# Optimization experiments

Measured on AMD Instinct MI355X. Metric: run time of the kernel, lower is better.

The kernel has to match this reference:

```python
import jax, jax.numpy as jnp
import numpy as np

H = 8        # num_heads
LN_EPS = 1e-5
NEG = -1000000.0


def setup_inputs() -> dict:
    key = jax.random.key(0)
    ks = jax.random.split(key, 8)
    B, T, D = 4, 4096, 1024
    s = 1.0 / np.sqrt(D)
    x = jax.random.normal(ks[0], (B, T, D), dtype=jnp.float32)
    tmask = (jnp.arange(T) < (3 * T) // 4).astype(jnp.float32)
    src_mask = jnp.broadcast_to(tmask[None, :, None], (B, T, 1)).astype(jnp.float32)
    Wq = jax.random.normal(ks[1], (D, D), dtype=jnp.float32) * s
    Wk = jax.random.normal(ks[2], (D, D), dtype=jnp.float32) * s
    Wv = jax.random.normal(ks[3], (D, D), dtype=jnp.float32) * s
    bq = jnp.zeros((D,), jnp.float32)
    bk = jnp.zeros((D,), jnp.float32)
    bv = jnp.zeros((D,), jnp.float32)
    gamma = jnp.ones((D,), jnp.float32)
    beta = jnp.zeros((D,), jnp.float32)
    return {"x": x, "src_mask": src_mask, "Wq": Wq, "bq": bq, "Wk": Wk,
            "bk": bk, "Wv": Wv, "bv": bv, "gamma": gamma, "beta": beta}


def reference(x, src_mask, Wq, bq, Wk, bk, Wv, bv, gamma, beta):
    B, T, D = x.shape
    Dh = D // H
    # LayerNorm (same normed input feeds q, k, v)
    mu = jnp.mean(x, axis=-1, keepdims=True)
    var = jnp.mean(jnp.square(x - mu), axis=-1, keepdims=True)
    xn = (x - mu) * jax.lax.rsqrt(var + LN_EPS) * gamma + beta
    q = xn @ Wq + bq                               # [B,T,D]
    k = xn @ Wk + bk + (1.0 - src_mask) * NEG      # mask padded timesteps
    v = (xn @ Wv + bv) * src_mask                  # zero padded values
    q = jax.nn.softmax(q.reshape(B, T, H, Dh), axis=-1)   # over feature dim
    k = jax.nn.softmax(k.reshape(B, T, H, Dh), axis=1)    # over time dim
    v = v.reshape(B, T, H, Dh)
    # efficient/linear attention: O(T * Dh^2) per head
    att = jnp.einsum('bnhd,bnhl->bhdl', k, v)      # [B,H,Dh,Dh]
    y = jnp.einsum('bnhd,bhdl->bnhl', q, att).reshape(B, T, D)
    return x + y
```

## Files before the change

### kernel.cpp

```cpp
#include <hip/hip_runtime.h>
#include <stdint.h>


typedef unsigned short u16;
typedef __attribute__((ext_vector_type(8))) short bf16x8;
typedef __attribute__((ext_vector_type(4))) float f32x4;

__device__ u16 g_WT[3][1024 * 1024];
__device__ u16 g_xn[16777216];
__device__ u16 g_ekT[16777216];
__device__ u16 g_vvT[16777216];
__device__ float g_attp[8388608];
__device__ u16 g_attT[524288];
__device__ float g_Z[4096];

__device__ __forceinline__ float b2f(u16 u) {
  union { unsigned int i; float f; } c;
  c.i = ((unsigned int)u) << 16;
  return c.f;
}
__device__ __forceinline__ u16 f2b(float f) {
  union { float f; unsigned int i; } c;
  c.f = f;
  unsigned int r = c.i + 0x7fffu + ((c.i >> 16) & 1u);
  return (u16)(r >> 16);
}

__device__ __forceinline__ void gload16(const void* g, void* l) {
  __builtin_amdgcn_global_load_lds(
      reinterpret_cast<const __attribute__((address_space(1))) uint32_t*>(
          reinterpret_cast<uintptr_t>(g)),
      reinterpret_cast<__attribute__((address_space(3))) uint32_t*>(
          reinterpret_cast<uintptr_t>(l)),
      16, 0, 0);
}

__device__ __forceinline__ void stage128x32(const u16* g, int stride, char* lds,
                                            int wave, int lane) {
  const int r = wave * 32 + (lane >> 2);
  const int cb = (lane & 3) * 16;
  const char* gp = (const char*)g;
  gload16(gp + (size_t)r * stride * 2 + cb, lds + wave * 2048);
  gload16(gp + (size_t)(r + 16) * stride * 2 + cb, lds + wave * 2048 + 1024);
}

__device__ __forceinline__ bf16x8 frag_ld(const char* lds, int row, int lane) {
  return *(const bf16x8*)(lds + row * 64 + ((lane >> 4) * 16));
}

__device__ __forceinline__ void tile_mfma(const char* As, const char* Bs,
                                          f32x4 (&acc)[4][4], int wm, int wn,
                                          int lane) {
  bf16x8 af[4], bfr[4];
#pragma unroll
  for (int i = 0; i < 4; i++) af[i] = frag_ld(As, wm * 64 + i * 16 + (lane & 15), lane);
#pragma unroll
  for (int j = 0; j < 4; j++) bfr[j] = frag_ld(Bs, wn * 64 + j * 16 + (lane & 15), lane);
#pragma unroll
  for (int i = 0; i < 4; i++)
#pragma unroll
    for (int j = 0; j < 4; j++)
      acc[i][j] = __builtin_amdgcn_mfma_f32_16x16x32_bf16(af[i], bfr[j], acc[i][j], 0, 0, 0);
}

__global__ __launch_bounds__(256) void prep_kernel(const float* __restrict__ x,
                                                   const float* __restrict__ gamma,
                                                   const float* __restrict__ beta,
                                                   const float* __restrict__ wq,
                                                   const float* __restrict__ wk,
                                                   const float* __restrict__ wv) {
  __shared__ float ls[4], ls2[4];
  __shared__ u16 tile[32][33];
  const int bid = blockIdx.x;
  const int tid = threadIdx.x;
  if (bid < 16384) {
    if (bid < 16) g_Z[bid * 256 + tid] = 0.0f;
    const int wave = tid >> 6, lane = tid & 63;
    const float* xr = x + (size_t)bid * 1024;
    float4 u = ((const float4*)xr)[tid];
    float v0 = u.x, v1 = u.y, v2 = u.z, v3 = u.w;
    float s = v0 + v1 + v2 + v3;
    float s2 = v0 * v0 + v1 * v1 + v2 * v2 + v3 * v3;
#pragma unroll
    for (int off = 32; off > 0; off >>= 1) {
      s += __shfl_down(s, off);
      s2 += __shfl_down(s2, off);
    }
    if (lane == 0) { ls[wave] = s; ls2[wave] = s2; }
    __syncthreads();
    s = ls[0] + ls[1] + ls[2] + ls[3];
    s2 = ls2[0] + ls2[1] + ls2[2] + ls2[3];
    const float mu = s * (1.0f / 1024.0f);
    const float var = fmaxf(s2 * (1.0f / 1024.0f) - mu * mu, 0.0f);
    const float rstd = rsqrtf(var + 1e-5f);
    float4 g4 = ((const float4*)gamma)[tid];
    float4 be = ((const float4*)beta)[tid];
    ushort4 o;
    o.x = f2b((v0 - mu) * rstd * g4.x + be.x);
    o.y = f2b((v1 - mu) * rstd * g4.y + be.y);
    o.z = f2b((v2 - mu) * rstd * g4.z + be.z);
    o.w = f2b((v3 - mu) * rstd * g4.w + be.w);
    *(ushort4*)(g_xn + (size_t)bid * 1024 + tid * 4) = o;
  } else {
    const int id = bid - 16384;
    const int which = id >> 10;
    const int rem = id & 1023;
    const float* src = (which == 0) ? wq : (which == 1) ? wk : wv;
    u16* dst = g_WT[which];
    const int tx = tid & 31;
    const int ty = tid >> 5;
    const int c0 = (rem & 31) * 32, r0 = (rem >> 5) * 32;
#pragma unroll
    for (int i = 0; i < 4; i++)
      tile[ty + i * 8][tx] = f2b(src[(size_t)(r0 + ty + i * 8) * 1024 + c0 + tx]);
    __syncthreads();
#pragma unroll
    for (int i = 0; i < 4; i++)
      dst[(size_t)(c0 + ty + i * 8) * 1024 + r0 + tx] = tile[tx][ty + i * 8];
  }
}

__global__ __launch_bounds__(256) void gemm_kv(const float* __restrict__ bk,
                                               const float* __restrict__ bv,
                                               const float* __restrict__ mask) {
  __shared__ __align__(16) char smem[34816];
  char* A0 = smem;
  char* B0 = smem + 8192;
  char* A1 = smem + 16384;
  char* B1 = smem + 24576;
  u16* tT = (u16*)smem;
  const int tid = threadIdx.x, wave = tid >> 6, lane = tid & 63;
  const int L = blockIdx.x;
  const int c = L & 7;
  const int k = L >> 3;
  const int inner = k & 15;
  const int n0 = (inner & 7) * 128;
  const int z = inner >> 3;
  const int m0 = (c + 8 * (k >> 4)) * 128;
  const u16* wt = z ? g_WT[2] : g_WT[1];
  const float* bias = z ? bv : bk;
  u16* outT = z ? g_vvT : g_ekT;
  const int b = m0 >> 12;
  const int t0 = m0 & 4095;
  const int wm = wave & 1, wn = wave >> 1;
  const u16* Ag = g_xn + (size_t)m0 * 1024;
  const u16* Bg = wt + (size_t)n0 * 1024;

  f32x4 zero = {0.f, 0.f, 0.f, 0.f};
  f32x4 acc[4][4];
#pragma unroll
  for (int i = 0; i < 4; i++)
#pragma unroll
    for (int j = 0; j < 4; j++) acc[i][j] = zero;

  stage128x32(Ag, 1024, A0, wave, lane);
  stage128x32(Bg, 1024, B0, wave, lane);
  __syncthreads();
  for (int k0 = 0; k0 < 1024; k0 += 64) {
    stage128x32(Ag + k0 + 32, 1024, A1, wave, lane);
    stage128x32(Bg + k0 + 32, 1024, B1, wave, lane);
    tile_mfma(A0, B0, acc, wm, wn, lane);
    __syncthreads();
    if (k0 + 64 < 1024) {
      stage128x32(Ag + k0 + 64, 1024, A0, wave, lane);
      stage128x32(Bg + k0 + 64, 1024, B0, wave, lane);
    }
    tile_mfma(A1, B1, acc, wm, wn, lane);
    __syncthreads();
  }

  float fsum[4] = {0.f, 0.f, 0.f, 0.f};
#pragma unroll
  for (int i = 0; i < 4; i++)
#pragma unroll
    for (int r = 0; r < 4; r++) {
      const int rowl = wm * 64 + i * 16 + (lane >> 4) * 4 + r;
      const float mv = mask[m0 + rowl];
#pragma unroll
      for (int j = 0; j < 4; j++) {
        const int coll = wn * 64 + j * 16 + (lane & 15);
        const float a = acc[i][j][r] + bias[n0 + coll];
        float o;
        if (z)
          o = a * mv;
        else
          o = (mv > 0.5f) ? __expf(fminf(a, 30.0f)) : 0.0f;
        const u16 ob = f2b(o);
        tT[coll * 136 + rowl] = ob;
        if (!z) fsum[j] += b2f(ob);
      }
    }
  if (!z) {
#pragma unroll
    for (int j = 0; j < 4; j++) {
      float s = fsum[j];
      s += __shfl_xor(s, 16);
      s += __shfl_xor(s, 32);
      if (lane < 16) atomicAdd(&g_Z[b * 1024 + n0 + wn * 64 + j * 16 + lane], s);
    }
  }
  __syncthreads();
  const size_t gbase = (size_t)b * (1024 * 4096) + (size_t)n0 * 4096 + t0;
#pragma unroll
  for (int u = 0; u < 8; u++) {
    const int v = u * 256 + tid;
    const int cc = v >> 4, rb = (v & 15) * 8;
    uint4 val = *(const uint4*)&tT[cc * 136 + rb];
    *(uint4*)(outT + gbase + (size_t)cc * 4096 + rb) = val;
  }
}

__global__ __launch_bounds__(256) void gemm_att() {
  __shared__ __align__(16) char smem[32768];
  char* A0 = smem;
  char* B0 = smem + 8192;
  char* A1 = smem + 16384;
  char* B1 = smem + 24576;
  const int tid = threadIdx.x, wave = tid >> 6, lane = tid & 63;
  const int kc = blockIdx.x;
  const int bh = blockIdx.y;
  const int b = bh >> 3, h = bh & 7;
  const size_t base = (size_t)b * (1024 * 4096) + (size_t)(h * 128) * 4096;
  const int wm = wave & 1, wn = wave >> 1;
  const u16* Ag = g_ekT + base + kc * 256;
  const u16* Bg = g_vvT + base + kc * 256;

  f32x4 zero = {0.f, 0.f, 0.f, 0.f};
  f32x4 acc[4][4];
#pragma unroll
  for (int i = 0; i < 4; i++)
#pragma unroll
    for (int j = 0; j < 4; j++) acc[i][j] = zero;

  stage128x32(Ag, 4096, A0, wave, lane);
  stage128x32(Bg, 4096, B0, wave, lane);
  __syncthreads();
  for (int kt = 0; kt < 256; kt += 64) {
    stage128x32(Ag + kt + 32, 4096, A1, wave, lane);
    stage128x32(Bg + kt + 32, 4096, B1, wave, lane);
    tile_mfma(A0, B0, acc, wm, wn, lane);
    __syncthreads();
    if (kt + 64 < 256) {
      stage128x32(Ag + kt + 64, 4096, A0, wave, lane);
      stage128x32(Bg + kt + 64, 4096, B0, wave, lane);
    }
    tile_mfma(A1, B1, acc, wm, wn, lane);
    __syncthreads();
  }

  float* op = g_attp + ((size_t)(kc * 32 + bh)) * 16384;
#pragma unroll
  for (int i = 0; i < 4; i++)
#pragma unroll
    for (int r = 0; r < 4; r++) {
      const int row = wm * 64 + i * 16 + (lane >> 4) * 4 + r;
#pragma unroll
      for (int j = 0; j < 4; j++) {
        const int col = wn * 64 + j * 16 + (lane & 15);
        op[row * 128 + col] = acc[i][j][r];
      }
    }
}

__global__ __launch_bounds__(256) void attnorm_kernel() {
  const int bh = blockIdx.x;
  const int b = bh >> 3, h = bh & 7;
  const int tid = threadIdx.x;
  __shared__ float Zl[128];
  if (tid < 128) Zl[tid] = fmaxf(g_Z[b * 1024 + h * 128 + tid], 1e-30f);
  __syncthreads();
  const int i0 = blockIdx.y * 2048;
  for (int i = i0 + tid; i < i0 + 2048; i += 256) {
    const int d = i >> 7, l = i & 127;
    float s = 0.f;
#pragma unroll
    for (int c = 0; c < 16; c++) s += g_attp[((size_t)(c * 32 + bh)) * 16384 + i];
    g_attT[(size_t)bh * 16384 + l * 128 + d] = f2b(s / Zl[d]);
  }
}

__global__ __launch_bounds__(256) void gemm_qy(const float* __restrict__ bq,
                                               const float* __restrict__ x,
                                               float* __restrict__ out) {
  __shared__ __align__(16) char smem[51200];
  __shared__ float zqp[2][128];
  char* A0 = smem;
  char* B0 = smem + 8192;
  char* A1 = smem + 16384;
  char* B1 = smem + 24576;
  u16* qs = (u16*)smem;
  char* C0 = smem + 34816;
  char* C1 = smem + 43008;
  const int tid = threadIdx.x, wave = tid >> 6, lane = tid & 63;
  const int L = blockIdx.x;
  const int c = L & 7;
  const int k = L >> 3;
  const int h = k & 7;
  const int m0 = (c + 8 * (k >> 3)) * 128;
  const int b = m0 >> 12;
  const int bh = b * 8 + h;
  const int wm = wave & 1, wn = wave >> 1;
  const u16* Ag = g_xn + (size_t)m0 * 1024;
  const u16* Bg = g_WT[0] + (size_t)(h * 128) * 1024;
  const u16* Cg = g_attT + (size_t)bh * 16384;

  f32x4 zero = {0.f, 0.f, 0.f, 0.f};
  f32x4 acc[4][4];
#pragma unroll
  for (int i = 0; i < 4; i++)
#pragma unroll
    for (int j = 0; j < 4; j++) acc[i][j] = zero;

  stage128x32(Ag, 1024, A0, wave, lane);
  stage128x32(Bg, 1024, B0, wave, lane);
  __syncthreads();
  for (int k0 = 0; k0 < 1024; k0 += 64) {
    stage128x32(Ag + k0 + 32, 1024, A1, wave, lane);
    stage128x32(Bg + k0 + 32, 1024, B1, wave, lane);
    tile_mfma(A0, B0, acc, wm, wn, lane);
    __syncthreads();
    if (k0 + 64 < 1024) {
      stage128x32(Ag + k0 + 64, 1024, A0, wave, lane);
      stage128x32(Bg + k0 + 64, 1024, B0, wave, lane);
    }
    tile_mfma(A1, B1, acc, wm, wn, lane);
    __syncthreads();
  }

  stage128x32(Cg, 128, C0, wave, lane);

#pragma unroll
  for (int i = 0; i < 4; i++)
#pragma unroll
    for (int r = 0; r < 4; r++) {
      const int rowl = wm * 64 + i * 16 + (lane >> 4) * 4 + r;
      float rs = 0.f;
#pragma unroll
      for (int j = 0; j < 4; j++) {
        const int coll = wn * 64 + j * 16 + (lane & 15);
        const float e = __expf(fminf(acc[i][j][r] + bq[h * 128 + coll], 30.0f));
        qs[rowl * 136 + coll] = f2b(e);
        rs += e;
      }
      rs += __shfl_xor(rs, 1);
      rs += __shfl_xor(rs, 2);
      rs += __shfl_xor(rs, 4);
      rs += __shfl_xor(rs, 8);
      if ((lane & 15) == 0) zqp[wn][rowl] = rs;
    }
  __syncthreads();

  f32x4 acc2[4][4];
#pragma unroll
  for (int i = 0; i < 4; i++)
#pragma unroll
    for (int j = 0; j < 4; j++) acc2[i][j] = zero;

  for (int k0 = 0; k0 < 128; k0 += 64) {
    stage128x32(Cg + k0 + 32, 128, C1, wave, lane);
    {
      bf16x8 af[4], bfr[4];
#pragma unroll
      for (int i = 0; i < 4; i++)
        af[i] = *(const bf16x8*)&qs[(wm * 64 + i * 16 + (lane & 15)) * 136 + k0 + (lane >> 4) * 8];
#pragma unroll
      for (int j = 0; j < 4; j++) bfr[j] = frag_ld(C0, wn * 64 + j * 16 + (lane & 15), lane);
#pragma unroll
      for (int i = 0; i < 4; i++)
#pragma unroll
        for (int j = 0; j < 4; j++)
          acc2[i][j] = __builtin_amdgcn_mfma_f32_16x16x32_bf16(af[i], bfr[j], acc2[i][j], 0, 0, 0);
    }
    __syncthreads();
    if (k0 + 64 < 128) stage128x32(Cg + k0 + 64, 128, C0, wave, lane);
    {
      bf16x8 af[4], bfr[4];
#pragma unroll
      for (int i = 0; i < 4; i++)
        af[i] = *(const bf16x8*)&qs[(wm * 64 + i * 16 + (lane & 15)) * 136 + k0 + 32 + (lane >> 4) * 8];
#pragma unroll
      for (int j = 0; j < 4; j++) bfr[j] = frag_ld(C1, wn * 64 + j * 16 + (lane & 15), lane);
#pragma unroll
      for (int i = 0; i < 4; i++)
#pragma unroll
        for (int j = 0; j < 4; j++)
          acc2[i][j] = __builtin_amdgcn_mfma_f32_16x16x32_bf16(af[i], bfr[j], acc2[i][j], 0, 0, 0);
    }
    __syncthreads();
  }

#pragma unroll
  for (int i = 0; i < 4; i++)
#pragma unroll
    for (int r = 0; r < 4; r++) {
      const int rowl = wm * 64 + i * 16 + (lane >> 4) * 4 + r;
      const float zq = fmaxf(zqp[0][rowl] + zqp[1][rowl], 1e-30f);
      const size_t n = (size_t)m0 + rowl;
#pragma unroll
      for (int j = 0; j < 4; j++) {
        const int coll = wn * 64 + j * 16 + (lane & 15);
        const size_t idx = n * 1024 + h * 128 + coll;
        out[idx] = x[idx] + acc2[i][j][r] / zq;
      }
    }
}

extern "C" void kernel_launch(void* const* d_in, const int* in_sizes, int n_in,
                              void* d_out, int out_size, void* d_ws, size_t ws_size,
                              hipStream_t stream) {
  const float* x = (const float*)d_in[0];
  const float* mask = (const float*)d_in[1];
  const float* Wq = (const float*)d_in[2];
  const float* bq = (const float*)d_in[3];
  const float* Wk = (const float*)d_in[4];
  const float* bk = (const float*)d_in[5];
  const float* Wv = (const float*)d_in[6];
  const float* bv = (const float*)d_in[7];
  const float* gamma = (const float*)d_in[8];
  const float* beta = (const float*)d_in[9];
  float* out = (float*)d_out;
  (void)d_ws; (void)ws_size;

  prep_kernel<<<dim3(16384 + 3072), 256, 0, stream>>>(x, gamma, beta, Wq, Wk, Wv);
  gemm_kv<<<dim3(2048), 256, 0, stream>>>(bk, bv, mask);
  gemm_att<<<dim3(16, 32), 256, 0, stream>>>();
  attnorm_kernel<<<dim3(32, 8), 256, 0, stream>>>();
  gemm_qy<<<dim3(1024), 256, 0, stream>>>(bq, x, out);
}
```

Before: 378.0 us.

## Rewrite K/V GEMM with 256x256 tiles, 8 waves, swizzled LDS, pipelined stages

The K/V projection GEMM moves from 128x128 tiles with 4 waves to 256x256 tiles with 8 waves (512 threads). It uses 128 KB of XOR-swizzled shared memory, double-buffered with explicit vmcnt waits, barriers and setprio around interleaved MFMA phases. The aim is more operand reuse per loaded byte, fewer LDS bank conflicts, and loads overlapped with MFMA work. The cost is much higher LDS and register use per block, lower occupancy, and 512 blocks that may fill the GPU's CUs less evenly.

```diff
diff --git a/kernel.cpp b/kernel.cpp
--- a/kernel.cpp
+++ b/kernel.cpp
@@ -61,6 +61,35 @@
 #pragma unroll
     for (int j = 0; j < 4; j++)
       acc[i][j] = __builtin_amdgcn_mfma_f32_16x16x32_bf16(af[i], bfr[j], acc[i][j], 0, 0, 0);
+}
+
+__device__ __forceinline__ void stageA256(char* buf, const u16* gsrc, int h,
+                                          int wave, int lane) {
+#pragma unroll
+  for (int i = 0; i < 2; i++) {
+    const int ib = i * 64 + wave * 8;
+    const int rowb = (ib & 63) | ((ib & 64) << 1) | (h << 6);
+    const int row = rowb + (lane >> 3);
+    const int cc = (lane & 7) ^ (row & 7);
+    gload16((const char*)gsrc + ((size_t)row * 1024 + cc * 8) * 2,
+            buf + rowb * 128);
+  }
+}
+__device__ __forceinline__ void stageB256(char* buf, const u16* gsrc, int h,
+                                          int wave, int lane) {
+#pragma unroll
+  for (int i = 0; i < 2; i++) {
+    const int ib = i * 64 + wave * 8;
+    const int rowb = (ib & 31) | ((ib & 96) << 1) | (h << 5);
+    const int row = rowb + (lane >> 3);
+    const int cc = (lane & 7) ^ (row & 7);
+    gload16((const char*)gsrc + ((size_t)row * 1024 + cc * 8) * 2,
+            buf + rowb * 128);
+  }
+}
+__device__ __forceinline__ bf16x8 fragS(const char* buf, int R, int ks, int lane) {
+  const int q = lane >> 4;
+  return *(const bf16x8*)(buf + R * 128 + ((((ks << 2) + q) ^ (R & 7)) << 4));
 }
 
 __global__ __launch_bounds__(256) void prep_kernel(const float* __restrict__ x,
@@ -120,93 +149,190 @@
   }
 }
 
-__global__ __launch_bounds__(256) void gemm_kv(const float* __restrict__ bk,
-                                               const float* __restrict__ bv,
-                                               const float* __restrict__ mask) {
-  __shared__ __align__(16) char smem[34816];
-  char* A0 = smem;
-  char* B0 = smem + 8192;
-  char* A1 = smem + 16384;
-  char* B1 = smem + 24576;
-  u16* tT = (u16*)smem;
+__global__ __launch_bounds__(512, 2) void gemm_kv(const float* __restrict__ bk,
+                                                  const float* __restrict__ bv,
+                                                  const float* __restrict__ mask) {
+  __shared__ __align__(16) char smem[131072];
   const int tid = threadIdx.x, wave = tid >> 6, lane = tid & 63;
   const int L = blockIdx.x;
-  const int c = L & 7;
-  const int k = L >> 3;
-  const int inner = k & 15;
-  const int n0 = (inner & 7) * 128;
-  const int z = inner >> 3;
-  const int m0 = (c + 8 * (k >> 4)) * 128;
+  const int mt = (L & 7) + 8 * (L >> 6);
+  const int nt = (L >> 3) & 7;
+  const int n0 = (nt & 3) * 256;
+  const int z = nt >> 2;
+  const int m0 = mt * 256;
   const u16* wt = z ? g_WT[2] : g_WT[1];
   const float* bias = z ? bv : bk;
   u16* outT = z ? g_vvT : g_ekT;
   const int b = m0 >> 12;
   const int t0 = m0 & 4095;
-  const int wm = wave & 1, wn = wave >> 1;
+  const int wm = wave >> 2, wn = wave & 3;
   const u16* Ag = g_xn + (size_t)m0 * 1024;
   const u16* Bg = wt + (size_t)n0 * 1024;
 
   f32x4 zero = {0.f, 0.f, 0.f, 0.f};
-  f32x4 acc[4][4];
-#pragma unroll
-  for (int i = 0; i < 4; i++)
+  f32x4 acc[8][4];
+#pragma unroll
+  for (int i = 0; i < 8; i++)
 #pragma unroll
     for (int j = 0; j < 4; j++) acc[i][j] = zero;
-
-  stage128x32(Ag, 1024, A0, wave, lane);
-  stage128x32(Bg, 1024, B0, wave, lane);
-  __syncthreads();
-  for (int k0 = 0; k0 < 1024; k0 += 64) {
-    stage128x32(Ag + k0 + 32, 1024, A1, wave, lane);
-    stage128x32(Bg + k0 + 32, 1024, B1, wave, lane);
-    tile_mfma(A0, B0, acc, wm, wn, lane);
-    __syncthreads();
-    if (k0 + 64 < 1024) {
-      stage128x32(Ag + k0 + 64, 1024, A0, wave, lane);
-      stage128x32(Bg + k0 + 64, 1024, B0, wave, lane);
-    }
-    tile_mfma(A1, B1, acc, wm, wn, lane);
-    __syncthreads();
-  }
-
+  bf16x8 a[4][2], bB[2][2][2];
+
+  stageA256(smem, Ag, 0, wave, lane);
+  stageB256(smem + 65536, Bg, 0, wave, lane);
+  stageA256(smem, Ag, 1, wave, lane);
+  stageB256(smem + 65536, Bg, 1, wave, lane);
+  asm volatile("s_waitcnt vmcnt(0)" ::: "memory");
+  __builtin_amdgcn_s_barrier();
+
+#pragma unroll 1
+  for (int t = 0; t < 16; ++t) {
+    const int p = t & 1;
+    char* Ab = smem + p * 32768;
+    char* Bb = smem + 65536 + p * 32768;
+    char* An = smem + (p ^ 1) * 32768;
+    char* Bn = smem + 65536 + (p ^ 1) * 32768;
+    const u16* Agn = Ag + (t + 1) * 64;
+    const u16* Bgn = Bg + (t + 1) * 64;
+    const bool st = t < 15;
+
+#pragma unroll
+    for (int rf = 0; rf < 4; rf++) {
+      const int R = wm * 128 + rf * 16 + (lane & 15);
+#pragma unroll
+      for (int ks = 0; ks < 2; ks++) a[rf][ks] = fragS(Ab, R, ks, lane);
+    }
+#pragma unroll
+    for (int cf = 0; cf < 2; cf++) {
+      const int R = wn * 64 + cf * 16 + (lane & 15);
+#pragma unroll
+      for (int ks = 0; ks < 2; ks++) bB[0][cf][ks] = fragS(Bb, R, ks, lane);
+    }
+    if (st) {
+      stageA256(An, Agn, 0, wave, lane);
+      stageB256(Bn, Bgn, 0, wave, lane);
+      asm volatile("s_waitcnt vmcnt(4)" ::: "memory");
+    } else {
+      asm volatile("s_waitcnt vmcnt(0)" ::: "memory");
+    }
+    __builtin_amdgcn_s_barrier();
+    asm volatile("s_waitcnt lgkmcnt(0)" ::: "memory");
+    __builtin_amdgcn_sched_barrier(0);
+    __builtin_amdgcn_s_setprio(1);
+#pragma unroll
+    for (int rf = 0; rf < 4; rf++)
+#pragma unroll
+      for (int cf = 0; cf < 2; cf++)
+#pragma unroll
+        for (int ks = 0; ks < 2; ks++)
+          acc[rf][cf] = __builtin_amdgcn_mfma_f32_16x16x32_bf16(
+              a[rf][ks], bB[0][cf][ks], acc[rf][cf], 0, 0, 0);
+    __builtin_amdgcn_s_setprio(0);
+    __builtin_amdgcn_s_barrier();
+    __builtin_amdgcn_sched_barrier(0);
+
+#pragma unroll
+    for (int cf = 0; cf < 2; cf++) {
+      const int R = wn * 64 + 32 + cf * 16 + (lane & 15);
+#pragma unroll
+      for (int ks = 0; ks < 2; ks++) bB[1][cf][ks] = fragS(Bb, R, ks, lane);
+    }
+    if (st) stageB256(Bn, Bgn, 1, wave, lane);
+    __builtin_amdgcn_s_barrier();
+    asm volatile("s_waitcnt lgkmcnt(0)" ::: "memory");
+    __builtin_amdgcn_sched_barrier(0);
+    __builtin_amdgcn_s_setprio(1);
+#pragma unroll
+    for (int rf = 0; rf < 4; rf++)
+#pragma unroll
+      for (int cf = 0; cf < 2; cf++)
+#pragma unroll
+        for (int ks = 0; ks < 2; ks++)
+          acc[rf][2 + cf] = __builtin_amdgcn_mfma_f32_16x16x32_bf16(
+              a[rf][ks], bB[1][cf][ks], acc[rf][2 + cf], 0, 0, 0);
+    __builtin_amdgcn_s_setprio(0);
+    __builtin_amdgcn_s_barrier();
+    __builtin_amdgcn_sched_barrier(0);
+
+#pragma unroll
+    for (int rf = 0; rf < 4; rf++) {
+      const int R = wm * 128 + 64 + rf * 16 + (lane & 15);
+#pragma unroll
+      for (int ks = 0; ks < 2; ks++) a[rf][ks] = fragS(Ab, R, ks, lane);
+    }
+    if (st) stageA256(An, Agn, 1, wave, lane);
+    asm volatile("s_waitcnt vmcnt(4)" ::: "memory");
+    __builtin_amdgcn_s_barrier();
+    asm volatile("s_waitcnt lgkmcnt(0)" ::: "memory");
+    __builtin_amdgcn_sched_barrier(0);
+    __builtin_amdgcn_s_setprio(1);
+#pragma unroll
+    for (int rf = 0; rf < 4; rf++)
+#pragma unroll
+      for (int cf = 0; cf < 2; cf++)
+#pragma unroll
+        for (int ks = 0; ks < 2; ks++)
+          acc[4 + rf][2 + cf] = __builtin_amdgcn_mfma_f32_16x16x32_bf16(
+              a[rf][ks], bB[1][cf][ks], acc[4 + rf][2 + cf], 0, 0, 0);
+    __builtin_amdgcn_s_setprio(0);
+    __builtin_amdgcn_s_barrier();
+    __builtin_amdgcn_sched_barrier(0);
+
+    asm volatile("s_waitcnt vmcnt(2)" ::: "memory");
+    __builtin_amdgcn_s_barrier();
+    __builtin_amdgcn_s_setprio(1);
+#pragma unroll
+    for (int rf = 0; rf < 4; rf++)
+#pragma unroll
+      for (int cf = 0; cf < 2; cf++)
+#pragma unroll
+        for (int ks = 0; ks < 2; ks++)
+          acc[4 + rf][cf] = __builtin_amdgcn_mfma_f32_16x16x32_bf16(
+              a[rf][ks], bB[0][cf][ks], acc[4 + rf][cf], 0, 0, 0);
+    __builtin_amdgcn_s_setprio(0);
+    __builtin_amdgcn_s_barrier();
+    __builtin_amdgcn_sched_barrier(0);
+  }
+
+  u16* tT = (u16*)smem;
   float fsum[4] = {0.f, 0.f, 0.f, 0.f};
 #pragma unroll
-  for (int i = 0; i < 4; i++)
+  for (int rf = 0; rf < 8; rf++)
 #pragma unroll
     for (int r = 0; r < 4; r++) {
-      const int rowl = wm * 64 + i * 16 + (lane >> 4) * 4 + r;
-      const float mv = mask[m0 + rowl];
-#pragma unroll
-      for (int j = 0; j < 4; j++) {
-        const int coll = wn * 64 + j * 16 + (lane & 15);
-        const float a = acc[i][j][r] + bias[n0 + coll];
+      const int tok = wm * 128 + rf * 16 + (lane >> 4) * 4 + r;
+      const float mv = mask[m0 + tok];
+#pragma unroll
+      for (int cf = 0; cf < 4; cf++) {
+        const int feat = wn * 64 + cf * 16 + (lane & 15);
+        const float aV = acc[rf][cf][r] + bias[n0 + feat];
         float o;
         if (z)
-          o = a * mv;
+          o = aV * mv;
         else
-          o = (mv > 0.5f) ? __expf(fminf(a, 30.0f)) : 0.0f;
+          o = (mv > 0.5f) ? __expf(fminf(aV, 30.0f)) : 0.0f;
         const u16 ob = f2b(o);
-        tT[coll * 136 + rowl] = ob;
-        if (!z) fsum[j] += b2f(ob);
+        tT[feat * 256 + ((((tok >> 3) ^ (feat & 7)) << 3) | (tok & 7))] = ob;
+        if (!z) fsum[cf] += b2f(ob);
       }
     }
   if (!z) {
 #pragma unroll
-    for (int j = 0; j < 4; j++) {
-      float s = fsum[j];
+    for (int cf = 0; cf < 4; cf++) {
+      float s = fsum[cf];
       s += __shfl_xor(s, 16);
       s += __shfl_xor(s, 32);
-      if (lane < 16) atomicAdd(&g_Z[b * 1024 + n0 + wn * 64 + j * 16 + lane], s);
+      if (lane < 16)
+        atomicAdd(&g_Z[b * 1024 + n0 + wn * 64 + cf * 16 + lane], s);
     }
   }
   __syncthreads();
   const size_t gbase = (size_t)b * (1024 * 4096) + (size_t)n0 * 4096 + t0;
 #pragma unroll
-  for (int u = 0; u < 8; u++) {
-    const int v = u * 256 + tid;
-    const int cc = v >> 4, rb = (v & 15) * 8;
-    uint4 val = *(const uint4*)&tT[cc * 136 + rb];
-    *(uint4*)(outT + gbase + (size_t)cc * 4096 + rb) = val;
+  for (int u = 0; u < 16; u++) {
+    const int id = u * 512 + tid;
+    const int feat = id >> 5, c = id & 31;
+    uint4 val = *(const uint4*)&tT[feat * 256 + ((c ^ (feat & 7)) << 3)];
+    *(uint4*)(outT + gbase + (size_t)feat * 4096 + c * 8) = val;
   }
 }
 
@@ -422,7 +548,7 @@
   (void)d_ws; (void)ws_size;
 
   prep_kernel<<<dim3(16384 + 3072), 256, 0, stream>>>(x, gamma, beta, Wq, Wk, Wv);
-  gemm_kv<<<dim3(2048), 256, 0, stream>>>(bk, bv, mask);
+  gemm_kv<<<dim3(512), 512, 0, stream>>>(bk, bv, mask);
   gemm_att<<<dim3(16, 32), 256, 0, stream>>>();
   attnorm_kernel<<<dim3(32, 8), 256, 0, stream>>>();
   gemm_qy<<<dim3(1024), 256, 0, stream>>>(bq, x, out);
```

After: 335.4 us. 1.13x faster.
